# Kernel tuning notes

Hardware: AMD Instinct MI355X
Metric: run time of the kernel (lower is better)

## Reference

```python
import jax, jax.numpy as jnp
import numpy as np

B, S, D, V = 4, 1024, 512, 8192
SCALES = [1, 2, 4, 8, 16]   # nn.Parameter init; used via int(scale.item()) -> static
WIN = 8                     # min(8, S//2) in compute_semantic_coherence
EPS = 1e-5


def layer_norm(x, g, b):
    m = x.mean(-1, keepdims=True)
    v = ((x - m) ** 2).mean(-1, keepdims=True)
    return (x - m) / jnp.sqrt(v + EPS) * g + b


def setup_inputs() -> dict:
    key = jax.random.key(0)
    ks = jax.random.split(key, 24)
    n = lambda k, shape, s=0.02: (jax.random.normal(k, shape, jnp.float32) * s)
    return {
        "embeddings": jax.random.normal(ks[0], (B, S, D), jnp.float32),
        "token_ids": jax.random.randint(ks[1], (B, S), 0, V),
        "context_mask": jnp.ones((B, S), jnp.float32),
        "token_similarity": n(ks[2], (V, V)),
        "W_scale": n(ks[3], (len(SCALES), D), 0.05), "b_scale": jnp.zeros((D,), jnp.float32),
        "W_sem": n(ks[4], (1, D), 0.05), "b_sem": jnp.zeros((D,), jnp.float32),
        "W_ctx": n(ks[5], (D, D), 0.02), "b_ctx": jnp.zeros((D,), jnp.float32),
        "W_fuse": n(ks[6], (4 * D, D), 0.02), "b_fuse": jnp.zeros((D,), jnp.float32),
        "ln1_g": jnp.ones((D,), jnp.float32), "ln1_b": jnp.zeros((D,), jnp.float32),
        "ln2_g": jnp.ones((D,), jnp.float32), "ln2_b": jnp.zeros((D,), jnp.float32),
        "ln3_g": jnp.ones((D,), jnp.float32), "ln3_b": jnp.zeros((D,), jnp.float32),
        "W_e0": n(ks[7], (D, D), 0.02), "b_e0": jnp.zeros((D,), jnp.float32),
        "W_e1": n(ks[8], (D, D), 0.02), "b_e1": jnp.zeros((D,), jnp.float32),
        "W_e2": n(ks[9], (D, D), 0.02), "b_e2": jnp.zeros((D,), jnp.float32),
    }


def _forward(embeddings, token_ids, context_mask, token_similarity,
             W_scale, b_scale, W_sem, b_sem, W_ctx, b_ctx, W_fuse, b_fuse,
             ln1_g, ln1_b, ln2_g, ln2_b, ln3_g, ln3_b,
             W_e0, b_e0, W_e1, b_e1, W_e2, b_e2):
    phases = jnp.tanh(embeddings)  # [B,S,D]

    # --- multi-scale coherence via cumulative sums + cos angle-difference identity ---
    # mean_t cos(p_t - m) = cos(m)*mean(cos p) + sin(m)*mean(sin p) over each window
    z = jnp.zeros((B, 1, D), phases.dtype)
    cum_p = jnp.concatenate([z, jnp.cumsum(phases, 1)], 1)            # [B,S+1,D]
    cum_c = jnp.concatenate([z, jnp.cumsum(jnp.cos(phases), 1)], 1)
    cum_s = jnp.concatenate([z, jnp.cumsum(jnp.sin(phases), 1)], 1)
    cols = []
    for s in SCALES:
        wm = (cum_p[:, s:] - cum_p[:, :-s]) / s   # window mean  [B,S-s+1,D]
        ac = (cum_c[:, s:] - cum_c[:, :-s]) / s   # window mean cos
        asn = (cum_s[:, s:] - cum_s[:, :-s]) / s  # window mean sin
        coh = jnp.mean(jnp.cos(wm) * ac + jnp.sin(wm) * asn, -1)      # [B,S-s+1]
        cols.append(jnp.pad(coh, ((0, 0), (0, s - 1))))               # torch leaves tail zeros
    msc = jnp.stack(cols, -1)                                         # [B,S,num_scales]
    scale_coh = msc @ W_scale + b_scale                               # [B,S,D]

    # --- semantic coherence (windowed, sim-weighted; torch takes mean over WHOLE tensor incl. batch) ---
    te = token_similarity[token_ids]                                  # [B,S,V]
    ten = te / jnp.maximum(jnp.linalg.norm(te, axis=-1, keepdims=True), 1e-12)
    tsim = jnp.einsum('biv,bjv->bij', ten, ten)                       # [B,S,S]
    off = jnp.arange(-WIN, WIN + 1)
    pos = jnp.arange(S)[:, None] + off[None, :]                       # [S,17]
    valid = (pos >= 0) & (pos < S)
    posc = jnp.clip(pos, 0, S - 1)
    pwin = phases[:, posc]                                            # [B,S,17,D]
    swin = jnp.take_along_axis(tsim, jnp.broadcast_to(posc[None], (B, S, 2 * WIN + 1)), axis=2)
    coh = jnp.cos((phases[:, :, None, :] - pwin) * swin[..., None]) * valid[None, :, :, None].astype(phases.dtype)
    counts = valid.sum(1).astype(phases.dtype)                        # [S]
    sem = coh.sum((0, 2, 3)) / (B * counts * D)                       # [S] (same scalar for all batches)
    sem = jnp.broadcast_to(sem[None, :], (B, S))[..., None]           # [B,S,1]
    sem_coh = sem @ W_sem + b_sem                                     # [B,S,D]

    # --- context coherence (context_mask path) ---
    cmean = jnp.mean(embeddings * context_mask[..., None], 1, keepdims=True)
    ctx_coh = jnp.cos(embeddings - cmean) @ W_ctx + b_ctx

    # --- local coherence ---
    lc = jnp.cos(embeddings[:, 1:] - embeddings[:, :-1])
    lc = jnp.concatenate([lc, jnp.zeros((B, 1, D), embeddings.dtype)], 1)

    allc = jnp.concatenate([scale_coh, sem_coh, ctx_coh, lc], -1)     # [B,S,4D]
    x = layer_norm(allc @ W_fuse + b_fuse, ln1_g, ln1_b)
    x = jax.nn.gelu(x, approximate=False)                             # dropout = identity (eval)
    for W, bb in ((W_e0, b_e0), (W_e1, b_e1), (W_e2, b_e2)):
        r = x
        h = layer_norm(x, ln2_g, ln2_b) @ W + bb
        x = r + jax.nn.gelu(h, approximate=False) * 0.1
    return layer_norm(x, ln3_g, ln3_b)


def reference(embeddings, token_ids, context_mask, token_similarity,
              W_scale, b_scale, W_sem, b_sem, W_ctx, b_ctx, W_fuse, b_fuse,
              ln1_g, ln1_b, ln2_g, ln2_b, ln3_g, ln3_b,
              W_e0, b_e0, W_e1, b_e1, W_e2, b_e2):
    return _forward(embeddings, token_ids, context_mask, token_similarity,
                    W_scale, b_scale, W_sem, b_sem, W_ctx, b_ctx, W_fuse, b_fuse,
                    ln1_g, ln1_b, ln2_g, ln2_b, ln3_g, ln3_b,
                    W_e0, b_e0, W_e1, b_e1, W_e2, b_e2)
```

## Files before the change

### kernel.cpp

```cpp
#include <hip/hip_runtime.h>


#define DEV __device__ __forceinline__
typedef unsigned short u16;
typedef __bf16 bf16x8 __attribute__((ext_vector_type(8)));
typedef float f32x4 __attribute__((ext_vector_type(4)));

static constexpr int S = 1024;
static constexpr int D = 512;
static constexpr int KCAT = 1088;

DEV u16 f2bf(float f) {
  unsigned u = __float_as_uint(f);
  return (u16)((u + 0x7fffu + ((u >> 16) & 1u)) >> 16);
}
DEV float gelu(float x) { return 0.5f * x * (1.f + erff(x * 0.70710678118654752f)); }
DEV float wred(float v) {
#pragma unroll
  for (int off = 32; off; off >>= 1) v += __shfl_down(v, off, 64);
  return v;
}
DEV void bred2(float& a, float& b, float* sm, int tid) {
  a = wred(a); b = wred(b);
  int w = tid >> 6;
  if ((tid & 63) == 0) { sm[w] = a; sm[w + 4] = b; }
  __syncthreads();
  a = sm[0] + sm[1] + sm[2] + sm[3];
  b = sm[4] + sm[5] + sm[6] + sm[7];
  __syncthreads();
}
DEV float qred(float v) {
  v += __shfl_xor(v, 1, 64);
  v += __shfl_xor(v, 2, 64);
  return v;
}

static constexpr int CP = 132;
__global__ __launch_bounds__(256) void k_front(
    const float* __restrict__ emb, const float* __restrict__ mask,
    float* __restrict__ ph, float* __restrict__ cmacc,
    const float* __restrict__ sim, const int* __restrict__ tok,
    float* __restrict__ dots_raw, float* __restrict__ normsq,
    const float* __restrict__ W0, const float* __restrict__ W1,
    const float* __restrict__ W2, const float* __restrict__ Wf,
    const float* __restrict__ wctx, const float* __restrict__ Wsc,
    const float* __restrict__ Wsm, const float* __restrict__ bsc,
    const float* __restrict__ bsm, const float* __restrict__ bcx,
    u16* __restrict__ T0, u16* __restrict__ T1, u16* __restrict__ T2,
    u16* __restrict__ wcatT, float* __restrict__ ctx_acc,
    float* __restrict__ sm_acc) {
  __shared__ __align__(16) float smem[72 * CP];
  __shared__ int stok[72];
  int blk = blockIdx.x, tid = threadIdx.x;

  if (blk < 1024) {
    int bx = blk >> 4, cyb = blk & 15;
    int b = bx >> 4, g0 = (bx & 15) * 64, gidx = b * S + g0;
    if (tid < 72) {
      int p = g0 + tid;
      stok[tid] = (p < S) ? tok[b * S + p] : -1;
    }
    __syncthreads();
    const float4* sim4 = (const float4*)sim;
    int wave = tid >> 6, lane = tid & 63;
    f32x4 acc[9] = {};
    for (int cc = 0; cc < 4; ++cc) {
      int cy = cyb * 4 + cc;
#pragma unroll
      for (int it = 0; it < 9; ++it) {
        int u = it * 256 + tid, r = u >> 5, q = u & 31;
        int tk = stok[r];
        float4 v = make_float4(0.f, 0.f, 0.f, 0.f);
        if (tk >= 0) v = sim4[(size_t)tk * 2048 + cy * 32 + q];
        *(float4*)&smem[r * CP + 4 * q] = v;
      }
      __syncthreads();
      const float* base = &smem[lane * CP + wave * 32];
#pragma unroll 2
      for (int c4 = 0; c4 < 8; ++c4) {
        f32x4 va = *(const f32x4*)(base + 4 * c4);
        acc[8] += va * va;
#pragma unroll
        for (int o = 1; o <= 8; ++o) {
          f32x4 vb = *(const f32x4*)(base + o * CP + 4 * c4);
          acc[o - 1] += va * vb;
        }
      }
      __syncthreads();
    }
    float* red = smem;
#pragma unroll
    for (int s = 0; s < 9; ++s) {
      f32x4 a = acc[s];
      red[(wave * 9 + s) * 64 + lane] = a[0] + a[1] + a[2] + a[3];
    }
    __syncthreads();
    for (int u = tid; u < 576; u += 256) {
      int s = u >> 6, a = u & 63;
      float v = red[s * 64 + a] + red[(9 + s) * 64 + a] +
                red[(18 + s) * 64 + a] + red[(27 + s) * 64 + a];
      if (s < 8) atomicAdd(&dots_raw[(size_t)(gidx + a) * 8 + s], v);
      else       atomicAdd(&normsq[gidx + a], v);
    }
    return;
  }

  if (blk < 2080) {
    int blk2 = blk - 1024;
    if (blk2 < 1024) {
      int idx = blk2 * 256 + tid;
#pragma unroll
      for (int r = 0; r < 2; ++r, idx += 262144) {
        float4 v = ((const float4*)emb)[idx];
        float4 o;
        o.x = tanhf(v.x); o.y = tanhf(v.y); o.z = tanhf(v.z); o.w = tanhf(v.w);
        ((float4*)ph)[idx] = o;
      }
    } else {
      int r = blk2 - 1024, b = r >> 3, chunk = r & 7;
      float a0 = 0.f, a1 = 0.f;
      for (int s = chunk * 128; s < chunk * 128 + 128; ++s) {
        float m = mask[b * S + s];
        const float* row = emb + (size_t)(b * S + s) * D;
        a0 += row[tid] * m; a1 += row[tid + 256] * m;
      }
      atomicAdd(cmacc + b * D + tid, a0);
      atomicAdd(cmacc + b * D + tid + 256, a1);
    }
    return;
  }

  int blk2 = blk - 2080;
  if (blk2 < 256) {
    int z = blk2 >> 6, rem = blk2 & 63;
    const float* src = z == 0 ? W0 : z == 1 ? W1 : z == 2 ? W2 : Wf + (size_t)1536 * 512;
    int r0 = (rem >> 3) * 64, c0 = (rem & 7) * 64;
    int tr = tid >> 6, tc = tid & 63;
#pragma unroll 4
    for (int i = 0; i < 16; ++i)
      smem[(tr + i * 4) * 65 + tc] = src[(size_t)(r0 + tr + i * 4) * 512 + c0 + tc];
    __syncthreads();
#pragma unroll 4
    for (int i = 0; i < 16; ++i) {
      int n = c0 + tr + i * 4, k = r0 + tc;
      u16 v = f2bf(smem[tc * 65 + tr + i * 4]);
      if (z == 3) wcatT[(size_t)n * KCAT + 512 + k] = v;
      else (z == 0 ? T0 : z == 1 ? T1 : T2)[(size_t)n * 512 + k] = v;
    }
  } else if (blk2 < 512) {
    int rem = blk2 - 256;
    int n = (rem & 1) * 256 + tid;
    int kbase = ((rem & 63) >> 1) * 16;
    int j0 = (rem >> 6) * 128;
    float acc[16] = {};
    for (int j = j0; j < j0 + 128; ++j) {
      float wf3 = Wf[(size_t)(1024 + j) * 512 + n];
#pragma unroll
      for (int kk = 0; kk < 16; ++kk) acc[kk] += wctx[(size_t)(kbase + kk) * 512 + j] * wf3;
    }
#pragma unroll
    for (int kk = 0; kk < 16; ++kk)
      atomicAdd(&ctx_acc[(size_t)(kbase + kk) * 512 + n], acc[kk]);
  } else {
    int rem = blk2 - 512;
    int n = (rem & 1) * 256 + tid;
    int j0 = (rem >> 1) * 16;
    float a0 = 0.f, a1 = 0.f, a2 = 0.f, a3 = 0.f, a4 = 0.f, au = 0.f, ac = 0.f;
    for (int j = j0; j < j0 + 16; ++j) {
      float wf1 = Wf[(size_t)j * 512 + n];
      float wf2 = Wf[(size_t)(512 + j) * 512 + n];
      float wf3 = Wf[(size_t)(1024 + j) * 512 + n];
      a0 += Wsc[j] * wf1; a1 += Wsc[512 + j] * wf1; a2 += Wsc[1024 + j] * wf1;
      a3 += Wsc[1536 + j] * wf1; a4 += Wsc[2048 + j] * wf1;
      au += Wsm[j] * wf2;
      ac += bsc[j] * wf1 + bsm[j] * wf2 + bcx[j] * wf3;
    }
    atomicAdd(&sm_acc[0 * 512 + n], a0);
    atomicAdd(&sm_acc[1 * 512 + n], a1);
    atomicAdd(&sm_acc[2 * 512 + n], a2);
    atomicAdd(&sm_acc[3 * 512 + n], a3);
    atomicAdd(&sm_acc[4 * 512 + n], a4);
    atomicAdd(&sm_acc[5 * 512 + n], au);
    atomicAdd(&sm_acc[6 * 512 + n], ac);
  }
}

static constexpr int CP2 = 68;
__global__ __launch_bounds__(256) void k_mid(const float* __restrict__ ph,
    const float* __restrict__ dots_raw, const float* __restrict__ normsq,
    float* __restrict__ msc_raw, float* __restrict__ semacc,
    const float* __restrict__ ctx_acc, const float* __restrict__ sm_acc,
    const float* __restrict__ bfu, u16* __restrict__ wcatT) {
  __shared__ __align__(16) float smem[7072];
  int blk = blockIdx.x, tid = threadIdx.x;

  if (blk < 512) {
    float* sP = smem;
    float* sw2 = smem + 88 * CP2;
    int bx = blk >> 3, dy = blk & 7;
    int b = bx >> 4, g0 = (bx & 15) * 64;
    const float4* ph4 = (const float4*)ph;
#pragma unroll
    for (int it = 0; it < 6; ++it) {
      int u = it * 256 + tid;
      if (u < 1408) {
        int r = u >> 4, q = u & 15;
        int gr = g0 - 8 + r;
        gr = gr < 0 ? 0 : (gr > S - 1 ? S - 1 : gr);
        float4 v = ph4[(size_t)(b * S + gr) * 128 + dy * 16 + q];
        *(float4*)&sP[r * CP2 + 4 * q] = v;
      }
    }
    for (int u = tid; u < 1088; u += 256) {
      int a = u / 17, oi = u - a * 17;
      int i = g0 + a, o = oi - 8, j = i + o;
      int idx = b * S + i;
      float v = 0.f;
      if (j >= 0 && j < S) {
        if (o == 0) v = 1.f;
        else {
          float dr = (o > 0) ? dots_raw[(size_t)idx * 8 + o - 1]
                             : dots_raw[(size_t)(idx + o) * 8 + (-o - 1)];
          float ni = fmaxf(sqrtf(normsq[idx]), 1e-12f);
          float nj = fmaxf(sqrtf(normsq[idx + o]), 1e-12f);
          v = dr / (ni * nj);
        }
      }
      sw2[u] = v;
    }
    __syncthreads();
    int ar = tid >> 2, dq = tid & 3;
    int i = g0 + ar, idx = b * S + i;
    int jmax = S - 1 - i; if (jmax > 15) jmax = 15;
    float swr[17];
#pragma unroll
    for (int oi = 0; oi < 17; ++oi) swr[oi] = sw2[ar * 17 + oi];
    float a0 = 0.f, a1 = 0.f, a2 = 0.f, a3 = 0.f, a4 = 0.f, asem = 0.f;
#pragma unroll 2
    for (int dd = 0; dd < 16; ++dd) {
      int d = dq + 4 * dd;
      const float* pb = &sP[(ar + 8) * CP2 + d];
      float sp = 0.f, sc = 0.f, ss = 0.f;
#pragma unroll
      for (int j = 0; j < 16; ++j) {
        float x = (j <= jmax) ? pb[j * CP2] : 0.f;
        sp += x; sc += __cosf(x); ss += __sinf(x);
        if (j == 0) a0 += __cosf(sp) * sc + __sinf(sp) * ss;
        else if (j == 1)  { float wm = sp * 0.5f;    a1 += __cosf(wm) * (sc * 0.5f)    + __sinf(wm) * (ss * 0.5f); }
        else if (j == 3)  { float wm = sp * 0.25f;   a2 += __cosf(wm) * (sc * 0.25f)   + __sinf(wm) * (ss * 0.25f); }
        else if (j == 7)  { float wm = sp * 0.125f;  a3 += __cosf(wm) * (sc * 0.125f)  + __sinf(wm) * (ss * 0.125f); }
        else if (j == 15) { float wm = sp * 0.0625f; a4 += __cosf(wm) * (sc * 0.0625f) + __sinf(wm) * (ss * 0.0625f); }
      }
      float p0 = pb[0];
      const float* qb = &sP[ar * CP2 + d];
#pragma unroll
      for (int oi = 0; oi < 17; ++oi) {
        int j = i + oi - 8;
        bool valid = (j >= 0) && (j < S);
        float pj = qb[oi * CP2];
        asem += valid ? __cosf((p0 - pj) * swr[oi]) : 0.f;
      }
    }
    a0 = qred(a0); a1 = qred(a1); a2 = qred(a2); a3 = qred(a3); a4 = qred(a4);
    asem = qred(asem);
    if (dq == 0) {
      float* mr = msc_raw + (size_t)idx * 5;
      atomicAdd(mr + 0, a0); atomicAdd(mr + 1, a1); atomicAdd(mr + 2, a2);
      atomicAdd(mr + 3, a3); atomicAdd(mr + 4, a4);
      atomicAdd(semacc + i, asem);
    }
    return;
  }

  int blk2 = blk - 512;
  if (blk2 < 64) {
    int r0 = (blk2 >> 3) * 64, c0 = (blk2 & 7) * 64;
    int tr = tid >> 6, tc = tid & 63;
#pragma unroll 4
    for (int i = 0; i < 16; ++i)
      smem[(tr + i * 4) * 65 + tc] = ctx_acc[(size_t)(r0 + tr + i * 4) * 512 + c0 + tc];
    __syncthreads();
#pragma unroll 4
    for (int i = 0; i < 16; ++i)
      wcatT[(size_t)(c0 + tr + i * 4) * KCAT + r0 + tc] = f2bf(smem[tc * 65 + tr + i * 4]);
  } else {
    int n = (blk2 - 64) * 256 + tid;
    u16* row = wcatT + (size_t)n * KCAT;
#pragma unroll
    for (int s = 0; s < 6; ++s) row[1024 + s] = f2bf(sm_acc[s * 512 + n]);
    row[1030] = f2bf(sm_acc[6 * 512 + n] + bfu[n]);
    for (int k = 1031; k < KCAT; ++k) row[k] = 0;
  }
}

__global__ __launch_bounds__(256) void k_xcat(const float* __restrict__ emb,
    const float* __restrict__ cmacc, const float* __restrict__ msc_raw,
    const float* __restrict__ semacc, u16* __restrict__ xcat) {
  int idx = blockIdx.x, b = idx >> 10, i = idx & 1023, tid = threadIdx.x;
  const float* erow = emb + (size_t)idx * D;
  u16* orow = xcat + (size_t)idx * KCAT;
  for (int c = tid; c < KCAT; c += 256) {
    float v;
    if (c < 512) {
      v = __cosf(erow[c] - cmacc[b * D + c] * (1.f / 1024.f));
    } else if (c < 1024) {
      int d = c - 512;
      v = (i < S - 1) ? __cosf(erow[D + d] - erow[d]) : 0.f;
    } else if (c < 1029) {
      int s = c - 1024, req = (1 << s) - 1;
      v = (S - 1 - i >= req) ? msc_raw[(size_t)idx * 5 + s] * (1.f / 512.f) : 0.f;
    } else if (c == 1029) {
      int cnt = ((i < 8) ? i : 8) + ((S - 1 - i < 8) ? (S - 1 - i) : 8) + 1;
      v = semacc[i] / (4.f * (float)cnt * 512.f);
    } else if (c == 1030) {
      v = 1.f;
    } else v = 0.f;
    orow[c] = f2bf(v);
  }
}

__global__ __launch_bounds__(256) void k_gemm(const u16* __restrict__ A,
    const u16* __restrict__ BT, float* __restrict__ C,
    const float* __restrict__ bias, int K) {
  __shared__ __align__(16) u16 sA[64 * 72];
  __shared__ __align__(16) u16 sB[64 * 72];
  int tid = threadIdx.x, wave = tid >> 6, lane = tid & 63;
  int m0 = blockIdx.x * 64, n0 = blockIdx.y * 64;
  int lr = tid >> 2, lc = (tid & 3) * 8;
  int q8 = (lane >> 4) * 8, l15 = lane & 15;
  const u16* Ap = A + (size_t)(m0 + lr) * K + lc;
  const u16* Bp = BT + (size_t)(n0 + lr) * K + lc;
  uint4 ra0 = *(const uint4*)(Ap);
  uint4 ra1 = *(const uint4*)(Ap + 32);
  uint4 rb0 = *(const uint4*)(Bp);
  uint4 rb1 = *(const uint4*)(Bp + 32);
  f32x4 acc[4] = {};
  for (int k0 = 0; k0 < K; k0 += 64) {
    *(uint4*)&sA[lr * 72 + lc]      = ra0;
    *(uint4*)&sA[lr * 72 + lc + 32] = ra1;
    *(uint4*)&sB[lr * 72 + lc]      = rb0;
    *(uint4*)&sB[lr * 72 + lc + 32] = rb1;
    __syncthreads();
    if (k0 + 64 < K) {
      ra0 = *(const uint4*)(Ap + k0 + 64);
      ra1 = *(const uint4*)(Ap + k0 + 96);
      rb0 = *(const uint4*)(Bp + k0 + 64);
      rb1 = *(const uint4*)(Bp + k0 + 96);
    }
    int row = wave * 16 + l15;
    bf16x8 af0 = *(const bf16x8*)&sA[row * 72 + q8];
    bf16x8 af1 = *(const bf16x8*)&sA[row * 72 + 32 + q8];
#pragma unroll
    for (int f = 0; f < 4; ++f) {
      bf16x8 b0 = *(const bf16x8*)&sB[(f * 16 + l15) * 72 + q8];
      bf16x8 b1 = *(const bf16x8*)&sB[(f * 16 + l15) * 72 + 32 + q8];
      acc[f] = __builtin_amdgcn_mfma_f32_16x16x32_bf16(af0, b0, acc[f], 0, 0, 0);
      acc[f] = __builtin_amdgcn_mfma_f32_16x16x32_bf16(af1, b1, acc[f], 0, 0, 0);
    }
    __syncthreads();
  }
  int r0 = m0 + wave * 16 + (lane >> 4) * 4;
#pragma unroll
  for (int f = 0; f < 4; ++f) {
    int col = n0 + f * 16 + l15;
    float bv = bias ? bias[col] : 0.f;
#pragma unroll
    for (int r = 0; r < 4; ++r)
      C[(size_t)(r0 + r) * 512 + col] = acc[f][r] + bv;
  }
}

__global__ __launch_bounds__(256) void k_post_y1(const float* __restrict__ y,
    float* __restrict__ x, u16* __restrict__ t,
    const float* __restrict__ g1, const float* __restrict__ b1,
    const float* __restrict__ g2, const float* __restrict__ b2) {
  __shared__ float sm[8];
  int row = blockIdx.x, tid = threadIdx.x;
  size_t base = (size_t)row * 512;
  float v0 = y[base + tid], v1 = y[base + tid + 256];
  float s = v0 + v1, ss = v0 * v0 + v1 * v1;
  bred2(s, ss, sm, tid);
  float m = s * (1.f / 512.f);
  float inv = rsqrtf(ss * (1.f / 512.f) - m * m + 1e-5f);
  float x0 = gelu((v0 - m) * inv * g1[tid] + b1[tid]);
  float x1 = gelu((v1 - m) * inv * g1[tid + 256] + b1[tid + 256]);
  x[base + tid] = x0; x[base + tid + 256] = x1;
  s = x0 + x1; ss = x0 * x0 + x1 * x1;
  bred2(s, ss, sm, tid);
  m = s * (1.f / 512.f);
  inv = rsqrtf(ss * (1.f / 512.f) - m * m + 1e-5f);
  t[base + tid] = f2bf((x0 - m) * inv * g2[tid] + b2[tid]);
  t[base + tid + 256] = f2bf((x1 - m) * inv * g2[tid + 256] + b2[tid + 256]);
}

__global__ __launch_bounds__(256) void k_post_res(const float* __restrict__ h,
    float* __restrict__ x, u16* __restrict__ t, float* __restrict__ out,
    const float* __restrict__ g, const float* __restrict__ bb, int final_) {
  __shared__ float sm[8];
  int row = blockIdx.x, tid = threadIdx.x;
  size_t base = (size_t)row * 512;
  float x0 = x[base + tid] + 0.1f * gelu(h[base + tid]);
  float x1 = x[base + tid + 256] + 0.1f * gelu(h[base + tid + 256]);
  float s = x0 + x1, ss = x0 * x0 + x1 * x1;
  bred2(s, ss, sm, tid);
  float m = s * (1.f / 512.f);
  float inv = rsqrtf(ss * (1.f / 512.f) - m * m + 1e-5f);
  float n0 = (x0 - m) * inv * g[tid] + bb[tid];
  float n1 = (x1 - m) * inv * g[tid + 256] + bb[tid + 256];
  if (final_) {
    out[base + tid] = n0; out[base + tid + 256] = n1;
  } else {
    x[base + tid] = x0; x[base + tid + 256] = x1;
    t[base + tid] = f2bf(n0); t[base + tid + 256] = f2bf(n1);
  }
}

extern "C" void kernel_launch(void* const* d_in, const int* in_sizes, int n_in,
                              void* d_out, int out_size, void* d_ws, size_t ws_size,
                              hipStream_t stream) {
  const float* emb     = (const float*)d_in[0];
  const int*   tok     = (const int*)d_in[1];
  const float* mask    = (const float*)d_in[2];
  const float* sim     = (const float*)d_in[3];
  const float* W_scale = (const float*)d_in[4];
  const float* b_scale = (const float*)d_in[5];
  const float* W_sem   = (const float*)d_in[6];
  const float* b_sem   = (const float*)d_in[7];
  const float* W_ctx   = (const float*)d_in[8];
  const float* b_ctx   = (const float*)d_in[9];
  const float* W_fuse  = (const float*)d_in[10];
  const float* b_fuse  = (const float*)d_in[11];
  const float* ln1_g = (const float*)d_in[12], *ln1_b = (const float*)d_in[13];
  const float* ln2_g = (const float*)d_in[14], *ln2_b = (const float*)d_in[15];
  const float* ln3_g = (const float*)d_in[16], *ln3_b = (const float*)d_in[17];
  const float* W_e0 = (const float*)d_in[18], *b_e0 = (const float*)d_in[19];
  const float* W_e1 = (const float*)d_in[20], *b_e1 = (const float*)d_in[21];
  const float* W_e2 = (const float*)d_in[22], *b_e2 = (const float*)d_in[23];
  float* out = (float*)d_out;

  char* w = (char*)d_ws; size_t off = 0;
  auto alloc = [&](size_t bytes) { void* p = w + off; off += (bytes + 255) & ~(size_t)255; return p; };
  float* phases = (float*)alloc((size_t)4096 * 512 * 4);
  float* hbuf   = (float*)alloc((size_t)4096 * 512 * 4);
  float* xbuf   = (float*)alloc((size_t)4096 * 512 * 4);
  u16*   tbuf   = (u16*)  alloc((size_t)4096 * 512 * 2);
  u16*   xcat   = (u16*)  alloc((size_t)4096 * KCAT * 2);
  u16*   wcatT  = (u16*)  alloc((size_t)512 * KCAT * 2);
  u16*   We0T   = (u16*)  alloc((size_t)512 * 512 * 2);
  u16*   We1T   = (u16*)  alloc((size_t)512 * 512 * 2);
  u16*   We2T   = (u16*)  alloc((size_t)512 * 512 * 2);
  float* semacc   = (float*)alloc((size_t)1024 * 4);
  float* cmacc    = (float*)alloc((size_t)4 * 512 * 4);
  float* dots_raw = (float*)alloc((size_t)4096 * 8 * 4);
  float* normsq   = (float*)alloc((size_t)4096 * 4);
  float* msc_raw  = (float*)alloc((size_t)4096 * 5 * 4);
  float* ctx_acc  = (float*)alloc((size_t)512 * 512 * 4);
  float* sm_acc   = (float*)alloc((size_t)7 * 512 * 4);
  (void)ws_size; (void)in_sizes; (void)n_in; (void)out_size;

  size_t zbytes = (size_t)(1024 + 4 * 512 + 4096 * 8 + 4096 + 4096 * 5 + 512 * 512 + 7 * 512) * 4;
  hipMemsetAsync(semacc, 0, zbytes, stream);

  k_front<<<2656, 256, 0, stream>>>(emb, mask, phases, cmacc,
                                    sim, tok, dots_raw, normsq,
                                    W_e0, W_e1, W_e2, W_fuse, W_ctx,
                                    W_scale, W_sem, b_scale, b_sem, b_ctx,
                                    We0T, We1T, We2T, wcatT, ctx_acc, sm_acc);
  k_mid<<<578, 256, 0, stream>>>(phases, dots_raw, normsq, msc_raw, semacc,
                                 ctx_acc, sm_acc, b_fuse, wcatT);

  k_xcat<<<4096, 256, 0, stream>>>(emb, cmacc, msc_raw, semacc, xcat);
  k_gemm<<<dim3(64, 8), 256, 0, stream>>>(xcat, wcatT, hbuf, nullptr, KCAT);
  k_post_y1<<<4096, 256, 0, stream>>>(hbuf, xbuf, tbuf, ln1_g, ln1_b, ln2_g, ln2_b);

  k_gemm<<<dim3(64, 8), 256, 0, stream>>>(tbuf, We0T, hbuf, b_e0, 512);
  k_post_res<<<4096, 256, 0, stream>>>(hbuf, xbuf, tbuf, nullptr, ln2_g, ln2_b, 0);
  k_gemm<<<dim3(64, 8), 256, 0, stream>>>(tbuf, We1T, hbuf, b_e1, 512);
  k_post_res<<<4096, 256, 0, stream>>>(hbuf, xbuf, tbuf, nullptr, ln2_g, ln2_b, 0);
  k_gemm<<<dim3(64, 8), 256, 0, stream>>>(tbuf, We2T, hbuf, b_e2, 512);
  k_post_res<<<4096, 256, 0, stream>>>(hbuf, xbuf, nullptr, out, ln3_g, ln3_b, 1);
}
```

Baseline: 589.8 us.

## Register-block sim dot-products, wave-per-row layernorms, bf16 residual GEMM outputs

```diff
diff --git a/kernel.cpp b/kernel.cpp
--- a/kernel.cpp
+++ b/kernel.cpp
@@ -14,20 +14,12 @@
   unsigned u = __float_as_uint(f);
   return (u16)((u + 0x7fffu + ((u >> 16) & 1u)) >> 16);
 }
+DEV float bf2f(u16 v) { return __uint_as_float((unsigned)v << 16); }
 DEV float gelu(float x) { return 0.5f * x * (1.f + erff(x * 0.70710678118654752f)); }
-DEV float wred(float v) {
-#pragma unroll
-  for (int off = 32; off; off >>= 1) v += __shfl_down(v, off, 64);
+DEV float wredx(float v) {
+#pragma unroll
+  for (int m = 32; m; m >>= 1) v += __shfl_xor(v, m, 64);
   return v;
-}
-DEV void bred2(float& a, float& b, float* sm, int tid) {
-  a = wred(a); b = wred(b);
-  int w = tid >> 6;
-  if ((tid & 63) == 0) { sm[w] = a; sm[w + 4] = b; }
-  __syncthreads();
-  a = sm[0] + sm[1] + sm[2] + sm[3];
-  b = sm[4] + sm[5] + sm[6] + sm[7];
-  __syncthreads();
 }
 DEV float qred(float v) {
   v += __shfl_xor(v, 1, 64);
@@ -35,7 +27,6 @@
   return v;
 }
 
-static constexpr int CP = 132;
 __global__ __launch_bounds__(256) void k_front(
     const float* __restrict__ emb, const float* __restrict__ mask,
     float* __restrict__ ph, float* __restrict__ cmacc,
@@ -49,7 +40,7 @@
     u16* __restrict__ T0, u16* __restrict__ T1, u16* __restrict__ T2,
     u16* __restrict__ wcatT, float* __restrict__ ctx_acc,
     float* __restrict__ sm_acc) {
-  __shared__ __align__(16) float smem[72 * CP];
+  __shared__ __align__(16) float smem[9360];
   __shared__ int stok[72];
   int blk = blockIdx.x, tid = threadIdx.x;
 
@@ -57,13 +48,20 @@
     int bx = blk >> 4, cyb = blk & 15;
     int b = bx >> 4, g0 = (bx & 15) * 64, gidx = b * S + g0;
     if (tid < 72) {
-      int p = g0 + tid;
-      stok[tid] = (p < S) ? tok[b * S + p] : -1;
+      int pp = g0 + tid;
+      stok[tid] = (pp < S) ? tok[b * S + pp] : -1;
     }
     __syncthreads();
     const float4* sim4 = (const float4*)sim;
+    f32x4* sT4 = (f32x4*)smem;
     int wave = tid >> 6, lane = tid & 63;
-    f32x4 acc[9] = {};
+    int p = lane & 31, h = lane >> 5;
+    int qb = wave * 8 + h * 4;
+    const f32x4* bj[10];
+#pragma unroll
+    for (int j = 0; j < 10; ++j)
+      bj[j] = sT4 + (p + (j >> 1)) * 65 + 2 * qb + (j & 1);
+    f32x4 ac0[9] = {}, ac1[9] = {};
     for (int cc = 0; cc < 4; ++cc) {
       int cy = cyb * 4 + cc;
 #pragma unroll
@@ -72,33 +70,42 @@
         int tk = stok[r];
         float4 v = make_float4(0.f, 0.f, 0.f, 0.f);
         if (tk >= 0) v = sim4[(size_t)tk * 2048 + cy * 32 + q];
-        *(float4*)&smem[r * CP + 4 * q] = v;
+        f32x4 vv = {v.x, v.y, v.z, v.w};
+        sT4[(r >> 1) * 65 + 2 * q + (r & 1)] = vv;
       }
       __syncthreads();
-      const float* base = &smem[lane * CP + wave * 32];
-#pragma unroll 2
-      for (int c4 = 0; c4 < 8; ++c4) {
-        f32x4 va = *(const f32x4*)(base + 4 * c4);
-        acc[8] += va * va;
-#pragma unroll
-        for (int o = 1; o <= 8; ++o) {
-          f32x4 vb = *(const f32x4*)(base + o * CP + 4 * c4);
-          acc[o - 1] += va * vb;
-        }
+#pragma unroll
+      for (int c4 = 0; c4 < 4; ++c4) {
+        f32x4 v0 = bj[0][2 * c4], v1 = bj[1][2 * c4], v2 = bj[2][2 * c4],
+              v3 = bj[3][2 * c4], v4 = bj[4][2 * c4], v5 = bj[5][2 * c4],
+              v6 = bj[6][2 * c4], v7 = bj[7][2 * c4], v8 = bj[8][2 * c4],
+              v9 = bj[9][2 * c4];
+        ac0[8] += v0 * v0;  ac1[8] += v1 * v1;
+        ac0[0] += v0 * v1;  ac1[0] += v1 * v2;
+        ac0[1] += v0 * v2;  ac1[1] += v1 * v3;
+        ac0[2] += v0 * v3;  ac1[2] += v1 * v4;
+        ac0[3] += v0 * v4;  ac1[3] += v1 * v5;
+        ac0[4] += v0 * v5;  ac1[4] += v1 * v6;
+        ac0[5] += v0 * v6;  ac1[5] += v1 * v7;
+        ac0[6] += v0 * v7;  ac1[6] += v1 * v8;
+        ac0[7] += v0 * v8;  ac1[7] += v1 * v9;
       }
       __syncthreads();
     }
     float* red = smem;
 #pragma unroll
     for (int s = 0; s < 9; ++s) {
-      f32x4 a = acc[s];
-      red[(wave * 9 + s) * 64 + lane] = a[0] + a[1] + a[2] + a[3];
+      f32x4 a = ac0[s], c = ac1[s];
+      red[(wave * 9 + s) * 128 + h * 64 + 2 * p]     = a[0] + a[1] + a[2] + a[3];
+      red[(wave * 9 + s) * 128 + h * 64 + 2 * p + 1] = c[0] + c[1] + c[2] + c[3];
     }
     __syncthreads();
     for (int u = tid; u < 576; u += 256) {
       int s = u >> 6, a = u & 63;
-      float v = red[s * 64 + a] + red[(9 + s) * 64 + a] +
-                red[(18 + s) * 64 + a] + red[(27 + s) * 64 + a];
+      float v = 0.f;
+#pragma unroll
+      for (int wh = 0; wh < 8; ++wh)
+        v += red[((wh >> 1) * 9 + s) * 128 + (wh & 1) * 64 + a];
       if (s < 8) atomicAdd(&dots_raw[(size_t)(gidx + a) * 8 + s], v);
       else       atomicAdd(&normsq[gidx + a], v);
     }
@@ -320,8 +327,8 @@
 }
 
 __global__ __launch_bounds__(256) void k_gemm(const u16* __restrict__ A,
-    const u16* __restrict__ BT, float* __restrict__ C,
-    const float* __restrict__ bias, int K) {
+    const u16* __restrict__ BT, float* __restrict__ Cf, u16* __restrict__ Cb,
+    const float* __restrict__ bias, int K, int obf) {
   __shared__ __align__(16) u16 sA[64 * 72];
   __shared__ __align__(16) u16 sB[64 * 72];
   int tid = threadIdx.x, wave = tid >> 6, lane = tid & 63;
@@ -365,8 +372,11 @@
     int col = n0 + f * 16 + l15;
     float bv = bias ? bias[col] : 0.f;
 #pragma unroll
-    for (int r = 0; r < 4; ++r)
-      C[(size_t)(r0 + r) * 512 + col] = acc[f][r] + bv;
+    for (int r = 0; r < 4; ++r) {
+      float cv = acc[f][r] + bv;
+      if (obf) Cb[(size_t)(r0 + r) * 512 + col] = f2bf(cv);
+      else     Cf[(size_t)(r0 + r) * 512 + col] = cv;
+    }
   }
 }
 
@@ -374,44 +384,83 @@
     float* __restrict__ x, u16* __restrict__ t,
     const float* __restrict__ g1, const float* __restrict__ b1,
     const float* __restrict__ g2, const float* __restrict__ b2) {
-  __shared__ float sm[8];
-  int row = blockIdx.x, tid = threadIdx.x;
-  size_t base = (size_t)row * 512;
-  float v0 = y[base + tid], v1 = y[base + tid + 256];
-  float s = v0 + v1, ss = v0 * v0 + v1 * v1;
-  bred2(s, ss, sm, tid);
+  int tid = threadIdx.x, w = tid >> 6, lane = tid & 63;
+  int row = blockIdx.x * 4 + w;
+  size_t base = (size_t)row * 512 + lane * 8;
+  int gb = lane * 8;
+  float4 va = *(const float4*)(y + base);
+  float4 vb = *(const float4*)(y + base + 4);
+  float v[8] = {va.x, va.y, va.z, va.w, vb.x, vb.y, vb.z, vb.w};
+  float s = 0.f, ss = 0.f;
+#pragma unroll
+  for (int k = 0; k < 8; ++k) { s += v[k]; ss += v[k] * v[k]; }
+  s = wredx(s); ss = wredx(ss);
   float m = s * (1.f / 512.f);
   float inv = rsqrtf(ss * (1.f / 512.f) - m * m + 1e-5f);
-  float x0 = gelu((v0 - m) * inv * g1[tid] + b1[tid]);
-  float x1 = gelu((v1 - m) * inv * g1[tid + 256] + b1[tid + 256]);
-  x[base + tid] = x0; x[base + tid + 256] = x1;
-  s = x0 + x1; ss = x0 * x0 + x1 * x1;
-  bred2(s, ss, sm, tid);
-  m = s * (1.f / 512.f);
-  inv = rsqrtf(ss * (1.f / 512.f) - m * m + 1e-5f);
-  t[base + tid] = f2bf((x0 - m) * inv * g2[tid] + b2[tid]);
-  t[base + tid + 256] = f2bf((x1 - m) * inv * g2[tid + 256] + b2[tid + 256]);
-}
-
-__global__ __launch_bounds__(256) void k_post_res(const float* __restrict__ h,
+  float4 gA = *(const float4*)(g1 + gb), gB = *(const float4*)(g1 + gb + 4);
+  float4 bA = *(const float4*)(b1 + gb), bB = *(const float4*)(b1 + gb + 4);
+  float gv[8] = {gA.x, gA.y, gA.z, gA.w, gB.x, gB.y, gB.z, gB.w};
+  float bv[8] = {bA.x, bA.y, bA.z, bA.w, bB.x, bB.y, bB.z, bB.w};
+  float xv[8];
+  float s2 = 0.f, ss2 = 0.f;
+#pragma unroll
+  for (int k = 0; k < 8; ++k) {
+    xv[k] = gelu((v[k] - m) * inv * gv[k] + bv[k]);
+    s2 += xv[k]; ss2 += xv[k] * xv[k];
+  }
+  *(float4*)(x + base)     = make_float4(xv[0], xv[1], xv[2], xv[3]);
+  *(float4*)(x + base + 4) = make_float4(xv[4], xv[5], xv[6], xv[7]);
+  s2 = wredx(s2); ss2 = wredx(ss2);
+  m = s2 * (1.f / 512.f);
+  inv = rsqrtf(ss2 * (1.f / 512.f) - m * m + 1e-5f);
+  float4 g2A = *(const float4*)(g2 + gb), g2B = *(const float4*)(g2 + gb + 4);
+  float4 b2A = *(const float4*)(b2 + gb), b2B = *(const float4*)(b2 + gb + 4);
+  float g2v[8] = {g2A.x, g2A.y, g2A.z, g2A.w, g2B.x, g2B.y, g2B.z, g2B.w};
+  float b2v[8] = {b2A.x, b2A.y, b2A.z, b2A.w, b2B.x, b2B.y, b2B.z, b2B.w};
+  union { u16 us[8]; uint4 u4; } pk;
+#pragma unroll
+  for (int k = 0; k < 8; ++k) pk.us[k] = f2bf((xv[k] - m) * inv * g2v[k] + b2v[k]);
+  *(uint4*)(t + base) = pk.u4;
+}
+
+__global__ __launch_bounds__(256) void k_post_res(const u16* __restrict__ hb,
     float* __restrict__ x, u16* __restrict__ t, float* __restrict__ out,
     const float* __restrict__ g, const float* __restrict__ bb, int final_) {
-  __shared__ float sm[8];
-  int row = blockIdx.x, tid = threadIdx.x;
-  size_t base = (size_t)row * 512;
-  float x0 = x[base + tid] + 0.1f * gelu(h[base + tid]);
-  float x1 = x[base + tid + 256] + 0.1f * gelu(h[base + tid + 256]);
-  float s = x0 + x1, ss = x0 * x0 + x1 * x1;
-  bred2(s, ss, sm, tid);
+  int tid = threadIdx.x, w = tid >> 6, lane = tid & 63;
+  int row = blockIdx.x * 4 + w;
+  size_t base = (size_t)row * 512 + lane * 8;
+  int gb = lane * 8;
+  union { u16 us[8]; uint4 u4; } hk;
+  hk.u4 = *(const uint4*)(hb + base);
+  float4 xa = *(const float4*)(x + base);
+  float4 xb = *(const float4*)(x + base + 4);
+  float xv[8] = {xa.x, xa.y, xa.z, xa.w, xb.x, xb.y, xb.z, xb.w};
+  float s = 0.f, ss = 0.f;
+#pragma unroll
+  for (int k = 0; k < 8; ++k) {
+    xv[k] += 0.1f * gelu(bf2f(hk.us[k]));
+    s += xv[k]; ss += xv[k] * xv[k];
+  }
+  s = wredx(s); ss = wredx(ss);
   float m = s * (1.f / 512.f);
   float inv = rsqrtf(ss * (1.f / 512.f) - m * m + 1e-5f);
-  float n0 = (x0 - m) * inv * g[tid] + bb[tid];
-  float n1 = (x1 - m) * inv * g[tid + 256] + bb[tid + 256];
+  float4 gA = *(const float4*)(g + gb), gB = *(const float4*)(g + gb + 4);
+  float4 bA = *(const float4*)(bb + gb), bB = *(const float4*)(bb + gb + 4);
+  float gv[8] = {gA.x, gA.y, gA.z, gA.w, gB.x, gB.y, gB.z, gB.w};
+  float bv[8] = {bA.x, bA.y, bA.z, bA.w, bB.x, bB.y, bB.z, bB.w};
+  float nv[8];
+#pragma unroll
+  for (int k = 0; k < 8; ++k) nv[k] = (xv[k] - m) * inv * gv[k] + bv[k];
   if (final_) {
-    out[base + tid] = n0; out[base + tid + 256] = n1;
+    *(float4*)(out + base)     = make_float4(nv[0], nv[1], nv[2], nv[3]);
+    *(float4*)(out + base + 4) = make_float4(nv[4], nv[5], nv[6], nv[7]);
   } else {
-    x[base + tid] = x0; x[base + tid + 256] = x1;
-    t[base + tid] = f2bf(n0); t[base + tid + 256] = f2bf(n1);
+    *(float4*)(x + base)     = make_float4(xv[0], xv[1], xv[2], xv[3]);
+    *(float4*)(x + base + 4) = make_float4(xv[4], xv[5], xv[6], xv[7]);
+    union { u16 us[8]; uint4 u4; } pk;
+#pragma unroll
+    for (int k = 0; k < 8; ++k) pk.us[k] = f2bf(nv[k]);
+    *(uint4*)(t + base) = pk.u4;
   }
 }
 
@@ -444,6 +493,7 @@
   float* hbuf   = (float*)alloc((size_t)4096 * 512 * 4);
   float* xbuf   = (float*)alloc((size_t)4096 * 512 * 4);
   u16*   tbuf   = (u16*)  alloc((size_t)4096 * 512 * 2);
+  u16*   hb16   = (u16*)  alloc((size_t)4096 * 512 * 2);
   u16*   xcat   = (u16*)  alloc((size_t)4096 * KCAT * 2);
   u16*   wcatT  = (u16*)  alloc((size_t)512 * KCAT * 2);
   u16*   We0T   = (u16*)  alloc((size_t)512 * 512 * 2);
@@ -470,13 +520,13 @@
                                  ctx_acc, sm_acc, b_fuse, wcatT);
 
   k_xcat<<<4096, 256, 0, stream>>>(emb, cmacc, msc_raw, semacc, xcat);
-  k_gemm<<<dim3(64, 8), 256, 0, stream>>>(xcat, wcatT, hbuf, nullptr, KCAT);
-  k_post_y1<<<4096, 256, 0, stream>>>(hbuf, xbuf, tbuf, ln1_g, ln1_b, ln2_g, ln2_b);
-
-  k_gemm<<<dim3(64, 8), 256, 0, stream>>>(tbuf, We0T, hbuf, b_e0, 512);
-  k_post_res<<<4096, 256, 0, stream>>>(hbuf, xbuf, tbuf, nullptr, ln2_g, ln2_b, 0);
-  k_gemm<<<dim3(64, 8), 256, 0, stream>>>(tbuf, We1T, hbuf, b_e1, 512);
-  k_post_res<<<4096, 256, 0, stream>>>(hbuf, xbuf, tbuf, nullptr, ln2_g, ln2_b, 0);
-  k_gemm<<<dim3(64, 8), 256, 0, stream>>>(tbuf, We2T, hbuf, b_e2, 512);
-  k_post_res<<<4096, 256, 0, stream>>>(hbuf, xbuf, nullptr, out, ln3_g, ln3_b, 1);
-}
+  k_gemm<<<dim3(64, 8), 256, 0, stream>>>(xcat, wcatT, hbuf, nullptr, nullptr, KCAT, 0);
+  k_post_y1<<<1024, 256, 0, stream>>>(hbuf, xbuf, tbuf, ln1_g, ln1_b, ln2_g, ln2_b);
+
+  k_gemm<<<dim3(64, 8), 256, 0, stream>>>(tbuf, We0T, nullptr, hb16, b_e0, 512, 1);
+  k_post_res<<<1024, 256, 0, stream>>>(hb16, xbuf, tbuf, nullptr, ln2_g, ln2_b, 0);
+  k_gemm<<<dim3(64, 8), 256, 0, stream>>>(tbuf, We1T, nullptr, hb16, b_e1, 512, 1);
+  k_post_res<<<1024, 256, 0, stream>>>(hb16, xbuf, tbuf, nullptr, ln2_g, ln2_b, 0);
+  k_gemm<<<dim3(64, 8), 256, 0, stream>>>(tbuf, We2T, nullptr, hb16, b_e2, 512, 1);
+  k_post_res<<<1024, 256, 0, stream>>>(hb16, xbuf, nullptr, out, ln3_g, ln3_b, 1);
+}
```

Result: faster. 553.6 us (-6.1%).
